# Kernel tuning notes

Measured on AMD Instinct MI355X. Metric: run time of the kernel, lower is better.

The kernel has to match this reference:

```python
import jax, jax.numpy as jnp
import numpy as np

H = 16
D_IN = 1024
D_OUT = 1024
D_K = D_OUT // H
B = 8
S = 1024


def setup_inputs() -> dict:
    key = jax.random.key(0)
    ks = jax.random.split(key, 9)
    scale = 1.0 / np.sqrt(D_IN)
    inp = {
        "query": jax.random.normal(ks[0], (B, S, D_IN), dtype=jnp.float32),
        "key_": jax.random.normal(ks[1], (B, S, D_IN), dtype=jnp.float32),
        "value": jax.random.normal(ks[2], (B, S, D_IN), dtype=jnp.float32),
        "Wq": jax.random.uniform(ks[3], (D_OUT, D_IN), jnp.float32, -scale, scale),
        "bq": jax.random.uniform(ks[4], (D_OUT,), jnp.float32, -scale, scale),
        "Wk": jax.random.uniform(ks[5], (D_OUT, D_IN), jnp.float32, -scale, scale),
        "bk": jax.random.uniform(ks[6], (D_OUT,), jnp.float32, -scale, scale),
        "Wv": jax.random.uniform(ks[7], (D_OUT, D_IN), jnp.float32, -scale, scale),
        "bv": jax.random.uniform(ks[8], (D_OUT,), jnp.float32, -scale, scale),
    }
    return inp


def reference(query, key_, value, Wq, bq, Wk, bk, Wv, bv):
    batch = query.shape[0]

    def proj(x, W, b):
        # torch Linear: x @ W.T + b, then view(B, -1, h, d_k).transpose(1, 2)
        y = jnp.einsum("bsd,od->bso", x, W) + b
        return y.reshape(batch, -1, H, D_K).transpose(0, 2, 1, 3)  # [B, h, S, d_k]

    q = proj(query, Wq, bq)
    k = proj(key_, Wk, bk)
    v = proj(value, Wv, bv)

    scores = jnp.einsum("bhqd,bhkd->bhqk", q, k) / (D_K ** 0.5)  # [B, h, S, S]
    attn = jax.nn.softmax(scores, axis=-1)
    x = jnp.einsum("bhqk,bhkd->bhqd", attn, v)  # [B, h, S, d_k]

    # transpose(1, 2).contiguous().view(batch, -1) -> flatten seq*d_out
    return x.transpose(0, 2, 1, 3).reshape(batch, -1)
```

## Files before the change

kernel.cpp:

```cpp
#include <hip/hip_runtime.h>
#include <math.h>

#define NH   16
#define DK   64
#define SEQL 1024
#define NB   8
#define DIN  1024

typedef __bf16 bf16;
typedef __attribute__((ext_vector_type(8))) __bf16 bf16x8;
typedef __attribute__((ext_vector_type(4))) __bf16 bf16x4;
typedef __attribute__((ext_vector_type(4))) float f32x4;

#define QSCALE 0.18033688011112042f

static __device__ __forceinline__ f32x4 mfma_bf16(bf16x8 a, bf16x8 b, f32x4 c) {
  return __builtin_amdgcn_mfma_f32_16x16x32_bf16(a, b, c, 0, 0, 0);
}

static __device__ __forceinline__ void async16(const bf16* g, bf16* l) {
  __builtin_amdgcn_global_load_lds(
      (const __attribute__((address_space(1))) void*)g,
      (__attribute__((address_space(3))) void*)l, 16, 0, 0);
}

__global__ __launch_bounds__(256)
void cvt3_kernel(const float* __restrict__ s0, const float* __restrict__ s1,
                 const float* __restrict__ s2, bf16* __restrict__ d0,
                 bf16* __restrict__ d1, bf16* __restrict__ d2, int n8) {
  const int i = blockIdx.x * 256 + threadIdx.x;
  if (i >= n8) return;
  const float* s = (blockIdx.y == 0) ? s0 : (blockIdx.y == 1) ? s1 : s2;
  bf16*        d = (blockIdx.y == 0) ? d0 : (blockIdx.y == 1) ? d1 : d2;
  const f32x4* sp = (const f32x4*)s;
  const f32x4 a = sp[2 * i], b = sp[2 * i + 1];
  bf16x8 r;
  r[0] = (bf16)a[0]; r[1] = (bf16)a[1]; r[2] = (bf16)a[2]; r[3] = (bf16)a[3];
  r[4] = (bf16)b[0]; r[5] = (bf16)b[1]; r[6] = (bf16)b[2]; r[7] = (bf16)b[3];
  ((bf16x8*)d)[i] = r;
}

__global__ __launch_bounds__(256, 2)
void proj_kernel(const bf16* __restrict__ Xq, const bf16* __restrict__ Xk,
                 const bf16* __restrict__ Xv,
                 const bf16* __restrict__ Wq, const bf16* __restrict__ Wk,
                 const bf16* __restrict__ Wv,
                 const float* __restrict__ Bq, const float* __restrict__ Bk,
                 const float* __restrict__ Bv,
                 bf16* __restrict__ Yq, bf16* __restrict__ Yk,
                 bf16* __restrict__ Yv) {
  const int z = blockIdx.z;
  const bf16*  X  = (z == 0) ? Xq : (z == 1) ? Xk : Xv;
  const bf16*  W  = (z == 0) ? Wq : (z == 1) ? Wk : Wv;
  const float* Bi = (z == 0) ? Bq : (z == 1) ? Bk : Bv;
  bf16*        Y  = (z == 0) ? Yq : (z == 1) ? Yk : Yv;

  const int m0 = blockIdx.x * 128;
  const int n0 = blockIdx.y * 128;

  __shared__ __attribute__((aligned(16))) bf16 As[128 * 32];
  __shared__ __attribute__((aligned(16))) bf16 Bs[128 * 32];

  const int t    = threadIdx.x;
  const int l    = t & 63;
  const int w    = t >> 6;
  const int l15  = l & 15;
  const int quad = l >> 4;
  const int wm   = w & 1;
  const int wn   = w >> 1;

  f32x4 acc[4][4];
#pragma unroll
  for (int i = 0; i < 4; ++i)
#pragma unroll
    for (int j = 0; j < 4; ++j) acc[i][j] = (f32x4){0.f, 0.f, 0.f, 0.f};

  const int srow   = l >> 2;
  const int gchunk = (l & 3) ^ ((l >> 3) & 3);

  for (int k0 = 0; k0 < DIN; k0 += 32) {
    __syncthreads();
#pragma unroll
    for (int i = 0; i < 2; ++i) {
      const int slab = w * 32 + i * 16;
      const int r    = slab + srow;
      async16(X + (size_t)(m0 + r) * DIN + k0 + gchunk * 8, As + slab * 32);
      async16(W + (size_t)(n0 + r) * DIN + k0 + gchunk * 8, Bs + slab * 32);
    }
    __syncthreads();

    bf16x8 af[4], bfr[4];
    const int swz = quad ^ ((l15 >> 1) & 3);
#pragma unroll
    for (int mi = 0; mi < 4; ++mi)
      af[mi] = *(const bf16x8*)(As + (wm * 64 + mi * 16 + l15) * 32 + swz * 8);
#pragma unroll
    for (int nj = 0; nj < 4; ++nj)
      bfr[nj] = *(const bf16x8*)(Bs + (wn * 64 + nj * 16 + l15) * 32 + swz * 8);
#pragma unroll
    for (int mi = 0; mi < 4; ++mi)
#pragma unroll
      for (int nj = 0; nj < 4; ++nj)
        acc[mi][nj] = mfma_bf16(af[mi], bfr[nj], acc[mi][nj]);
  }

  if (z == 2) {
#pragma unroll
    for (int nj = 0; nj < 4; ++nj) {
      const int o    = n0 + wn * 64 + nj * 16 + l15;
      const float bv = Bi[o];
      const int h    = o >> 6;
      const int d    = o & 63;
#pragma unroll
      for (int mi = 0; mi < 4; ++mi) {
        const int m  = m0 + wm * 64 + mi * 16 + quad * 4;
        const int bl = m >> 10;
        const int s  = m & (SEQL - 1);
        bf16x4 pk;
#pragma unroll
        for (int r = 0; r < 4; ++r) pk[r] = (bf16)(acc[mi][nj][r] + bv);
        *(bf16x4*)(Y + ((size_t)(bl * NH + h) * DK + d) * SEQL + s) = pk;
      }
    }
  } else {
    const float scale = (z == 0) ? QSCALE : 1.0f;
#pragma unroll
    for (int nj = 0; nj < 4; ++nj) {
      const int o    = n0 + wn * 64 + nj * 16 + l15;
      const float bv = Bi[o];
      const int h    = o >> 6;
      const int d    = o & 63;
#pragma unroll
      for (int mi = 0; mi < 4; ++mi) {
#pragma unroll
        for (int r = 0; r < 4; ++r) {
          const int m  = m0 + wm * 64 + mi * 16 + quad * 4 + r;
          const int bl = m >> 10;
          const int s  = m & (SEQL - 1);
          Y[(size_t)(((bl * NH + h) << 10) | s) * DK + d] =
              (bf16)((acc[mi][nj][r] + bv) * scale);
        }
      }
    }
  }
}

__global__ __launch_bounds__(256, 2)
void attn_kernel(const bf16* __restrict__ Q, const bf16* __restrict__ K,
                 const bf16* __restrict__ V, float* __restrict__ Out, int b0) {
  const int bhl = blockIdx.x;
  const int q0  = blockIdx.y * 128;
  const int bg  = b0 + (bhl >> 4);
  const int h   = bhl & 15;
  const int t    = threadIdx.x;
  const int l    = t & 63;
  const int w    = t >> 6;
  const int l15  = l & 15;
  const int quad = l >> 4;

  const bf16* Qh = Q + (size_t)bhl * SEQL * DK;
  const bf16* Kh = K + (size_t)bhl * SEQL * DK;
  const bf16* Vh = V + (size_t)bhl * DK * SEQL;

  __shared__ __attribute__((aligned(16))) bf16 sKs[64 * 64];
  __shared__ __attribute__((aligned(16))) bf16 sVt[64 * 64];
  __shared__ __attribute__((aligned(16))) bf16 sPl[4][2][16 * 72];

  bf16x8 qf[2][2];
#pragma unroll
  for (int g = 0; g < 2; ++g)
#pragma unroll
    for (int hh = 0; hh < 2; ++hh)
      qf[g][hh] = *(const bf16x8*)(Qh + (size_t)(q0 + w * 32 + g * 16 + l15) * DK +
                                   hh * 32 + quad * 8);

  bf16x8 ones;
#pragma unroll
  for (int j = 0; j < 8; ++j) ones[j] = (bf16)1.0f;

  f32x4 oacc[2][4];
#pragma unroll
  for (int g = 0; g < 2; ++g)
#pragma unroll
    for (int n = 0; n < 4; ++n) oacc[g][n] = (f32x4){0.f, 0.f, 0.f, 0.f};
  f32x4 sacc[2];
  sacc[0] = (f32x4){0.f, 0.f, 0.f, 0.f};
  sacc[1] = (f32x4){0.f, 0.f, 0.f, 0.f};

  const int drow   = l >> 3;
  const int dchunk = l & 7;

  for (int kb = 0; kb < SEQL; kb += 64) {
    __syncthreads();
#pragma unroll
    for (int i = 0; i < 2; ++i) {
      const int r = w * 16 + i * 8 + drow;
      async16(Kh + (size_t)(kb + r) * DK + (dchunk ^ (r & 7)) * 8,
              sKs + (w * 16 + i * 8) * 64);
      async16(Vh + (size_t)r * SEQL + kb + (dchunk ^ (r & 7)) * 8,
              sVt + (w * 16 + i * 8) * 64);
    }
    __syncthreads();

    bf16x8 kf[4][2];
#pragma unroll
    for (int c = 0; c < 4; ++c)
#pragma unroll
      for (int hh = 0; hh < 2; ++hh)
        kf[c][hh] = *(const bf16x8*)(sKs + (c * 16 + l15) * 64 +
                                     (((hh * 4 + quad) ^ (l15 & 7)) * 8));

#pragma unroll
    for (int g = 0; g < 2; ++g) {
#pragma unroll
      for (int c = 0; c < 4; ++c) {
        f32x4 cs = (f32x4){0.f, 0.f, 0.f, 0.f};
        cs = mfma_bf16(kf[c][0], qf[g][0], cs);
        cs = mfma_bf16(kf[c][1], qf[g][1], cs);
        bf16x4 pk;
#pragma unroll
        for (int r = 0; r < 4; ++r) pk[r] = (bf16)exp2f(cs[r]);
        *(bf16x4*)(&sPl[w][g][l15 * 72 + c * 16 + quad * 4]) = pk;
      }
    }

    bf16x8 vfr[4][2];
#pragma unroll
    for (int n = 0; n < 4; ++n)
#pragma unroll
      for (int hh = 0; hh < 2; ++hh)
        vfr[n][hh] = *(const bf16x8*)(sVt + (n * 16 + l15) * 64 +
                                      (((hh * 4 + quad) ^ (l15 & 7)) * 8));
#pragma unroll
    for (int g = 0; g < 2; ++g) {
      const bf16x8 pf0 = *(const bf16x8*)(&sPl[w][g][l15 * 72 + quad * 8]);
      const bf16x8 pf1 = *(const bf16x8*)(&sPl[w][g][l15 * 72 + 32 + quad * 8]);
#pragma unroll
      for (int n = 0; n < 4; ++n) {
        oacc[g][n] = mfma_bf16(pf0, vfr[n][0], oacc[g][n]);
        oacc[g][n] = mfma_bf16(pf1, vfr[n][1], oacc[g][n]);
      }
      sacc[g] = mfma_bf16(pf0, ones, sacc[g]);
      sacc[g] = mfma_bf16(pf1, ones, sacc[g]);
    }
  }

#pragma unroll
  for (int g = 0; g < 2; ++g) {
    float linv[4];
#pragma unroll
    for (int r = 0; r < 4; ++r) linv[r] = 1.0f / sacc[g][r];
#pragma unroll
    for (int n = 0; n < 4; ++n) {
      const int d = n * 16 + l15;
#pragma unroll
      for (int r = 0; r < 4; ++r) {
        const int qrow = q0 + w * 32 + g * 16 + quad * 4 + r;
        Out[(size_t)((bg * SEQL + qrow) * NH + h) * DK + d] =
            oacc[g][n][r] * linv[r];
      }
    }
  }
}

extern "C" void kernel_launch(void* const* d_in, const int* in_sizes, int n_in,
                              void* d_out, int out_size, void* d_ws,
                              size_t ws_size, hipStream_t stream) {
  const float* q  = (const float*)d_in[0];
  const float* k  = (const float*)d_in[1];
  const float* v  = (const float*)d_in[2];
  const float* Wq = (const float*)d_in[3];
  const float* bq = (const float*)d_in[4];
  const float* Wk = (const float*)d_in[5];
  const float* bk = (const float*)d_in[6];
  const float* Wv = (const float*)d_in[7];
  const float* bv = (const float*)d_in[8];
  float* out = (float*)d_out;

  const size_t wElems = (size_t)DIN * DIN;
  const size_t wBytes = 3 * wElems * sizeof(bf16);
  const size_t perBatch = 6 * (size_t)SEQL * DIN * sizeof(bf16);
  int nbg = (ws_size > wBytes) ? (int)((ws_size - wBytes) / perBatch) : 1;
  if (nbg < 1) nbg = 1;
  if (nbg > NB) nbg = NB;

  bf16* Wqb = (bf16*)d_ws;
  bf16* Wkb = Wqb + wElems;
  bf16* Wvb = Wkb + wElems;
  const size_t g1 = (size_t)nbg * SEQL * DIN;
  bf16* Xqb = Wvb + wElems;
  bf16* Xkb = Xqb + g1;
  bf16* Xvb = Xkb + g1;
  bf16* Yqb = Xvb + g1;
  bf16* Ykb = Yqb + g1;
  bf16* Yvb = Ykb + g1;

  const int w8 = (int)(wElems / 8);
  dim3 gW((w8 + 255) / 256, 3);
  cvt3_kernel<<<gW, 256, 0, stream>>>(Wq, Wk, Wv, Wqb, Wkb, Wvb, w8);

  for (int b0 = 0; b0 < NB; b0 += nbg) {
    const int nb = (NB - b0 < nbg) ? (NB - b0) : nbg;
    const int n8 = nb * SEQL * DIN / 8;
    const size_t xoff = (size_t)b0 * SEQL * DIN;
    dim3 gX((n8 + 255) / 256, 3);
    cvt3_kernel<<<gX, 256, 0, stream>>>(q + xoff, k + xoff, v + xoff,
                                        Xqb, Xkb, Xvb, n8);

    dim3 gP(nb * 8, 8, 3);
    proj_kernel<<<gP, 256, 0, stream>>>(Xqb, Xkb, Xvb, Wqb, Wkb, Wvb,
                                        bq, bk, bv, Yqb, Ykb, Yvb);

    dim3 gA(nb * NH, SEQL / 128);
    attn_kernel<<<gA, 256, 0, stream>>>(Yqb, Ykb, Yvb, out, b0);
  }
}
```

Baseline: 284.0 us.

## Enlarge projection GEMM tiles to 256x256 with a double-buffered async LDS pipeline

The QKV projection GEMM moves from 128x128 tiles with K-step 32 and 256 threads to 256x256 tiles with K-step 64 and 512 threads. Operand tiles are double-buffered in LDS via async global-to-LDS loads, prefetched two K-tiles ahead. Each K-tile's MFMA work is split into four phases with explicit barriers, waitcnts and raised wave priority. The aim is more operand reuse per LDS byte and global loads that overlap with matrix math. The cost is 128KB of LDS per block and a much smaller grid, which may leave CUs unevenly loaded.

```diff
diff --git a/kernel.cpp b/kernel.cpp
--- a/kernel.cpp
+++ b/kernel.cpp
@@ -6,6 +6,7 @@
 #define SEQL 1024
 #define NB   8
 #define DIN  1024
+#define NKT  (DIN / 64)
 
 typedef __bf16 bf16;
 typedef __attribute__((ext_vector_type(8))) __bf16 bf16x8;
@@ -40,7 +41,7 @@
   ((bf16x8*)d)[i] = r;
 }
 
-__global__ __launch_bounds__(256, 2)
+__global__ __launch_bounds__(512, 2)
 void proj_kernel(const bf16* __restrict__ Xq, const bf16* __restrict__ Xk,
                  const bf16* __restrict__ Xv,
                  const bf16* __restrict__ Wq, const bf16* __restrict__ Wk,
@@ -55,54 +56,119 @@
   const float* Bi = (z == 0) ? Bq : (z == 1) ? Bk : Bv;
   bf16*        Y  = (z == 0) ? Yq : (z == 1) ? Yk : Yv;
 
-  const int m0 = blockIdx.x * 128;
-  const int n0 = blockIdx.y * 128;
-
-  __shared__ __attribute__((aligned(16))) bf16 As[128 * 32];
-  __shared__ __attribute__((aligned(16))) bf16 Bs[128 * 32];
+  const int m0 = blockIdx.x * 256;
+  const int n0 = blockIdx.y * 256;
+
+  __shared__ __attribute__((aligned(16))) bf16 sA[2][256 * 64];
+  __shared__ __attribute__((aligned(16))) bf16 sB[2][256 * 64];
 
   const int t    = threadIdx.x;
   const int l    = t & 63;
   const int w    = t >> 6;
   const int l15  = l & 15;
   const int quad = l >> 4;
-  const int wm   = w & 1;
-  const int wn   = w >> 1;
-
-  f32x4 acc[4][4];
-#pragma unroll
-  for (int i = 0; i < 4; ++i)
+  const int wm   = w >> 2;
+  const int wn   = w & 3;
+  const int axor = l15 & 7;
+
+  const int srow = l >> 3;
+  const int gcol = ((l & 7) ^ srow) * 8;
+
+  const bf16* Xb = X + (size_t)m0 * DIN;
+  const bf16* Wb = W + (size_t)n0 * DIN;
+
+  f32x4 acc[8][4];
+#pragma unroll
+  for (int i = 0; i < 8; ++i)
 #pragma unroll
     for (int j = 0; j < 4; ++j) acc[i][j] = (f32x4){0.f, 0.f, 0.f, 0.f};
 
-  const int srow   = l >> 2;
-  const int gchunk = (l & 3) ^ ((l >> 3) & 3);
-
-  for (int k0 = 0; k0 < DIN; k0 += 32) {
-    __syncthreads();
-#pragma unroll
-    for (int i = 0; i < 2; ++i) {
-      const int slab = w * 32 + i * 16;
-      const int r    = slab + srow;
-      async16(X + (size_t)(m0 + r) * DIN + k0 + gchunk * 8, As + slab * 32);
-      async16(W + (size_t)(n0 + r) * DIN + k0 + gchunk * 8, Bs + slab * 32);
-    }
-    __syncthreads();
-
-    bf16x8 af[4], bfr[4];
-    const int swz = quad ^ ((l15 >> 1) & 3);
-#pragma unroll
-    for (int mi = 0; mi < 4; ++mi)
-      af[mi] = *(const bf16x8*)(As + (wm * 64 + mi * 16 + l15) * 32 + swz * 8);
-#pragma unroll
-    for (int nj = 0; nj < 4; ++nj)
-      bfr[nj] = *(const bf16x8*)(Bs + (wn * 64 + nj * 16 + l15) * 32 + swz * 8);
-#pragma unroll
-    for (int mi = 0; mi < 4; ++mi)
-#pragma unroll
-      for (int nj = 0; nj < 4; ++nj)
-        acc[mi][nj] = mfma_bf16(af[mi], bfr[nj], acc[mi][nj]);
-  }
+#define STAGE(KT, BB)                                                        \
+  {                                                                          \
+    _Pragma("unroll")                                                        \
+    for (int c = 0; c < 4; ++c) {                                            \
+      const int rr = w * 32 + c * 8 + srow;                                  \
+      async16(Xb + (size_t)rr * DIN + (KT) * 64 + gcol,                      \
+              &sA[BB][(w * 4 + c) * 512]);                                   \
+      async16(Wb + (size_t)rr * DIN + (KT) * 64 + gcol,                      \
+              &sB[BB][(w * 4 + c) * 512]);                                   \
+    }                                                                        \
+  }
+
+#define PHASE_READS(RH, CH)                                                  \
+  bf16x8 af[4][2], bfr[2][2];                                                \
+  _Pragma("unroll")                                                          \
+  for (int fi = 0; fi < 4; ++fi) {                                           \
+    const int ra = wm * 128 + (RH) * 64 + fi * 16 + l15;                     \
+    _Pragma("unroll")                                                        \
+    for (int kh = 0; kh < 2; ++kh)                                           \
+      af[fi][kh] = *(const bf16x8*)(                                         \
+          &sA[b][ra * 64 + ((((kh << 2) | quad) ^ axor) << 3)]);             \
+  }                                                                          \
+  _Pragma("unroll")                                                          \
+  for (int fj = 0; fj < 2; ++fj) {                                           \
+    const int rb = wn * 64 + (CH) * 32 + fj * 16 + l15;                      \
+    _Pragma("unroll")                                                        \
+    for (int kh = 0; kh < 2; ++kh)                                           \
+      bfr[fj][kh] = *(const bf16x8*)(                                        \
+          &sB[b][rb * 64 + ((((kh << 2) | quad) ^ axor) << 3)]);             \
+  }
+
+#define PHASE_MFMA(RH, CH)                                                   \
+  _Pragma("unroll")                                                          \
+  for (int fi = 0; fi < 4; ++fi)                                             \
+    _Pragma("unroll")                                                        \
+    for (int fj = 0; fj < 2; ++fj) {                                         \
+      acc[(RH) * 4 + fi][(CH) * 2 + fj] = mfma_bf16(                         \
+          af[fi][0], bfr[fj][0], acc[(RH) * 4 + fi][(CH) * 2 + fj]);         \
+      acc[(RH) * 4 + fi][(CH) * 2 + fj] = mfma_bf16(                         \
+          af[fi][1], bfr[fj][1], acc[(RH) * 4 + fi][(CH) * 2 + fj]);         \
+    }
+
+#define PHASE(RH, CH)                                                        \
+  {                                                                          \
+    PHASE_READS(RH, CH)                                                      \
+    __builtin_amdgcn_s_barrier();                                            \
+    asm volatile("s_waitcnt lgkmcnt(0)" ::: "memory");                       \
+    __builtin_amdgcn_sched_barrier(0);                                       \
+    __builtin_amdgcn_s_setprio(1);                                           \
+    PHASE_MFMA(RH, CH)                                                       \
+    __builtin_amdgcn_s_setprio(0);                                           \
+    __builtin_amdgcn_s_barrier();                                            \
+  }
+
+  STAGE(0, 0)
+  STAGE(1, 1)
+  asm volatile("s_waitcnt vmcnt(8)" ::: "memory");
+  __builtin_amdgcn_s_barrier();
+
+  for (int kt = 0; kt < NKT; ++kt) {
+    const int b = kt & 1;
+    PHASE(0, 0)
+    PHASE(0, 1)
+    PHASE(1, 0)
+    {
+      PHASE_READS(1, 1)
+      asm volatile("s_waitcnt lgkmcnt(0)" ::: "memory");
+      __builtin_amdgcn_s_barrier();
+      __builtin_amdgcn_sched_barrier(0);
+      if (kt < NKT - 2) STAGE(kt + 2, b)
+      __builtin_amdgcn_s_setprio(1);
+      PHASE_MFMA(1, 1)
+      __builtin_amdgcn_s_setprio(0);
+      if (kt < NKT - 2) {
+        asm volatile("s_waitcnt vmcnt(8)" ::: "memory");
+      } else if (kt == NKT - 2) {
+        asm volatile("s_waitcnt vmcnt(0)" ::: "memory");
+      }
+      __builtin_amdgcn_s_barrier();
+    }
+  }
+
+#undef PHASE
+#undef PHASE_MFMA
+#undef PHASE_READS
+#undef STAGE
 
   if (z == 2) {
 #pragma unroll
@@ -112,8 +178,8 @@
       const int h    = o >> 6;
       const int d    = o & 63;
 #pragma unroll
-      for (int mi = 0; mi < 4; ++mi) {
-        const int m  = m0 + wm * 64 + mi * 16 + quad * 4;
+      for (int mi = 0; mi < 8; ++mi) {
+        const int m  = m0 + wm * 128 + mi * 16 + quad * 4;
         const int bl = m >> 10;
         const int s  = m & (SEQL - 1);
         bf16x4 pk;
@@ -131,10 +197,10 @@
       const int h    = o >> 6;
       const int d    = o & 63;
 #pragma unroll
-      for (int mi = 0; mi < 4; ++mi) {
+      for (int mi = 0; mi < 8; ++mi) {
 #pragma unroll
         for (int r = 0; r < 4; ++r) {
-          const int m  = m0 + wm * 64 + mi * 16 + quad * 4 + r;
+          const int m  = m0 + wm * 128 + mi * 16 + quad * 4 + r;
           const int bl = m >> 10;
           const int s  = m & (SEQL - 1);
           Y[(size_t)(((bl * NH + h) << 10) | s) * DK + d] =
@@ -307,8 +373,8 @@
     cvt3_kernel<<<gX, 256, 0, stream>>>(q + xoff, k + xoff, v + xoff,
                                         Xqb, Xkb, Xvb, n8);
 
-    dim3 gP(nb * 8, 8, 3);
-    proj_kernel<<<gP, 256, 0, stream>>>(Xqb, Xkb, Xvb, Wqb, Wkb, Wvb,
+    dim3 gP(nb * 4, 4, 3);
+    proj_kernel<<<gP, 512, 0, stream>>>(Xqb, Xkb, Xvb, Wqb, Wkb, Wvb,
                                         bq, bk, bv, Yqb, Ykb, Yvb);
 
     dim3 gA(nb * NH, SEQL / 128);
```

New measurement: 306.9 us. +8.1%, slower.

## Double attention query tile per block and fuse weight/input conversion launches

Applied to the files above, without the earlier changes.

The attention kernel now has each block cover 256 query rows, 64 per wave, instead of 128, so each staged K/V tile in shared memory serves twice as many queries. This halves K/V global reloads but doubles the accumulator and Q-fragment register footprint and halves the number of blocks. Separately, the weight conversion is merged with the input conversion into one six-way kernel launch. If the workspace forces more than one batch group, the weights are now reconverted on every iteration.

```diff
diff --git a/kernel.cpp b/kernel.cpp
--- a/kernel.cpp
+++ b/kernel.cpp
@@ -25,13 +25,21 @@
 }
 
 __global__ __launch_bounds__(256)
-void cvt3_kernel(const float* __restrict__ s0, const float* __restrict__ s1,
-                 const float* __restrict__ s2, bf16* __restrict__ d0,
-                 bf16* __restrict__ d1, bf16* __restrict__ d2, int n8) {
+void cvt6_kernel(const float* __restrict__ s0, const float* __restrict__ s1,
+                 const float* __restrict__ s2, const float* __restrict__ s3,
+                 const float* __restrict__ s4, const float* __restrict__ s5,
+                 bf16* __restrict__ d0, bf16* __restrict__ d1,
+                 bf16* __restrict__ d2, bf16* __restrict__ d3,
+                 bf16* __restrict__ d4, bf16* __restrict__ d5,
+                 int n8a, int n8b) {
+  const int y = blockIdx.y;
+  const int n8 = (y < 3) ? n8a : n8b;
   const int i = blockIdx.x * 256 + threadIdx.x;
   if (i >= n8) return;
-  const float* s = (blockIdx.y == 0) ? s0 : (blockIdx.y == 1) ? s1 : s2;
-  bf16*        d = (blockIdx.y == 0) ? d0 : (blockIdx.y == 1) ? d1 : d2;
+  const float* s = (y == 0) ? s0 : (y == 1) ? s1 : (y == 2) ? s2
+                 : (y == 3) ? s3 : (y == 4) ? s4 : s5;
+  bf16* d = (y == 0) ? d0 : (y == 1) ? d1 : (y == 2) ? d2
+          : (y == 3) ? d3 : (y == 4) ? d4 : d5;
   const f32x4* sp = (const f32x4*)s;
   const f32x4 a = sp[2 * i], b = sp[2 * i + 1];
   bf16x8 r;
@@ -149,7 +157,7 @@
 void attn_kernel(const bf16* __restrict__ Q, const bf16* __restrict__ K,
                  const bf16* __restrict__ V, float* __restrict__ Out, int b0) {
   const int bhl = blockIdx.x;
-  const int q0  = blockIdx.y * 128;
+  const int q0  = blockIdx.y * 256;
   const int bg  = b0 + (bhl >> 4);
   const int h   = bhl & 15;
   const int t    = threadIdx.x;
@@ -164,28 +172,28 @@
 
   __shared__ __attribute__((aligned(16))) bf16 sKs[64 * 64];
   __shared__ __attribute__((aligned(16))) bf16 sVt[64 * 64];
-  __shared__ __attribute__((aligned(16))) bf16 sPl[4][2][16 * 72];
-
-  bf16x8 qf[2][2];
-#pragma unroll
-  for (int g = 0; g < 2; ++g)
+  __shared__ __attribute__((aligned(16))) bf16 sPl[4][4][16 * 72];
+
+  bf16x8 qf[4][2];
+#pragma unroll
+  for (int g = 0; g < 4; ++g)
 #pragma unroll
     for (int hh = 0; hh < 2; ++hh)
-      qf[g][hh] = *(const bf16x8*)(Qh + (size_t)(q0 + w * 32 + g * 16 + l15) * DK +
+      qf[g][hh] = *(const bf16x8*)(Qh + (size_t)(q0 + w * 64 + g * 16 + l15) * DK +
                                    hh * 32 + quad * 8);
 
   bf16x8 ones;
 #pragma unroll
   for (int j = 0; j < 8; ++j) ones[j] = (bf16)1.0f;
 
-  f32x4 oacc[2][4];
-#pragma unroll
-  for (int g = 0; g < 2; ++g)
+  f32x4 oacc[4][4];
+#pragma unroll
+  for (int g = 0; g < 4; ++g)
 #pragma unroll
     for (int n = 0; n < 4; ++n) oacc[g][n] = (f32x4){0.f, 0.f, 0.f, 0.f};
-  f32x4 sacc[2];
-  sacc[0] = (f32x4){0.f, 0.f, 0.f, 0.f};
-  sacc[1] = (f32x4){0.f, 0.f, 0.f, 0.f};
+  f32x4 sacc[4];
+#pragma unroll
+  for (int g = 0; g < 4; ++g) sacc[g] = (f32x4){0.f, 0.f, 0.f, 0.f};
 
   const int drow   = l >> 3;
   const int dchunk = l & 7;
@@ -211,7 +219,7 @@
                                      (((hh * 4 + quad) ^ (l15 & 7)) * 8));
 
 #pragma unroll
-    for (int g = 0; g < 2; ++g) {
+    for (int g = 0; g < 4; ++g) {
 #pragma unroll
       for (int c = 0; c < 4; ++c) {
         f32x4 cs = (f32x4){0.f, 0.f, 0.f, 0.f};
@@ -232,7 +240,7 @@
         vfr[n][hh] = *(const bf16x8*)(sVt + (n * 16 + l15) * 64 +
                                       (((hh * 4 + quad) ^ (l15 & 7)) * 8));
 #pragma unroll
-    for (int g = 0; g < 2; ++g) {
+    for (int g = 0; g < 4; ++g) {
       const bf16x8 pf0 = *(const bf16x8*)(&sPl[w][g][l15 * 72 + quad * 8]);
       const bf16x8 pf1 = *(const bf16x8*)(&sPl[w][g][l15 * 72 + 32 + quad * 8]);
 #pragma unroll
@@ -246,7 +254,7 @@
   }
 
 #pragma unroll
-  for (int g = 0; g < 2; ++g) {
+  for (int g = 0; g < 4; ++g) {
     float linv[4];
 #pragma unroll
     for (int r = 0; r < 4; ++r) linv[r] = 1.0f / sacc[g][r];
@@ -255,7 +263,7 @@
       const int d = n * 16 + l15;
 #pragma unroll
       for (int r = 0; r < 4; ++r) {
-        const int qrow = q0 + w * 32 + g * 16 + quad * 4 + r;
+        const int qrow = q0 + w * 64 + g * 16 + quad * 4 + r;
         Out[(size_t)((bg * SEQL + qrow) * NH + h) * DK + d] =
             oacc[g][n][r] * linv[r];
       }
@@ -296,22 +304,24 @@
   bf16* Yvb = Ykb + g1;
 
   const int w8 = (int)(wElems / 8);
-  dim3 gW((w8 + 255) / 256, 3);
-  cvt3_kernel<<<gW, 256, 0, stream>>>(Wq, Wk, Wv, Wqb, Wkb, Wvb, w8);
 
   for (int b0 = 0; b0 < NB; b0 += nbg) {
     const int nb = (NB - b0 < nbg) ? (NB - b0) : nbg;
     const int n8 = nb * SEQL * DIN / 8;
     const size_t xoff = (size_t)b0 * SEQL * DIN;
-    dim3 gX((n8 + 255) / 256, 3);
-    cvt3_kernel<<<gX, 256, 0, stream>>>(q + xoff, k + xoff, v + xoff,
-                                        Xqb, Xkb, Xvb, n8);
+    const int xb = (n8 + 255) / 256;
+    const int wb = (w8 + 255) / 256;
+    dim3 gX((xb > wb) ? xb : wb, 6);
+    cvt6_kernel<<<gX, 256, 0, stream>>>(q + xoff, k + xoff, v + xoff,
+                                        Wq, Wk, Wv,
+                                        Xqb, Xkb, Xvb, Wqb, Wkb, Wvb,
+                                        n8, w8);
 
     dim3 gP(nb * 8, 8, 3);
     proj_kernel<<<gP, 256, 0, stream>>>(Xqb, Xkb, Xvb, Wqb, Wkb, Wvb,
                                         bq, bk, bv, Yqb, Ykb, Yvb);
 
-    dim3 gA(nb * NH, SEQL / 128);
+    dim3 gA(nb * NH, SEQL / 256);
     attn_kernel<<<gA, 256, 0, stream>>>(Yqb, Ykb, Yvb, out, b0);
   }
 }
```

After: 281.4 us. No clear change (-0.9%).
